# Kernel optimization log

Measured on AMD Instinct MI355X. Metric: run time of the kernel, lower is better.

Reference implementation:

```python
import jax, jax.numpy as jnp
import numpy as np

N, D, P = 4096, 1024, 2048
TAU, ALPHA = 0.2, 0.8
GAMMA_EX, GAMMA_IN = 2.0, 1.6
EPS = 1e-8


def _cos_sim(e):
    # F.cosine_similarity(e[:,None], e[None,:], dim=2) == normalized rows matmul
    n = jnp.linalg.norm(e, axis=1, keepdims=True)
    en = e / jnp.maximum(n, EPS)
    return en @ en.T  # [N, N]


def setup_inputs() -> dict:
    key = jax.random.key(0)
    embeddings = jax.random.normal(key, (N, D), dtype=jnp.float32)
    # positive pairs: (0,1),(2,3),... (arange fill)
    pp = np.arange(2 * P).reshape(P, 2)
    pos_partner = np.arange(N)
    pos_partner[pp[:, 0]] = pp[:, 1]
    pos_partner[pp[:, 1]] = pp[:, 0]
    # negative pairs = all ordered (i,j), i!=j, minus ordered positive tuples,
    # enumerated row-major (deterministic stand-in for torch's set order).
    pos_m = np.zeros((N, N), dtype=bool)
    pos_m[pp[:, 0], pp[:, 1]] = True
    neg_m = ~np.eye(N, dtype=bool) & ~pos_m
    ii, jj = np.nonzero(neg_m)  # row-major order
    neg_partner = np.arange(N)
    neg_partner[ii] = jj
    neg_partner[jj] = ii  # processed[j] = ... overwrites after
    return {
        "embeddings": embeddings,
        "positive_pairs": jnp.asarray(pp, jnp.int32),
        "pos_partner": jnp.asarray(pos_partner, jnp.int32),
        "neg_partner": jnp.asarray(neg_partner, jnp.int32),
    }


def reference(embeddings, positive_pairs, pos_partner, neg_partner):
    pi, pj = positive_pairs[:, 0], positive_pairs[:, 1]
    # Beta(gamma,gamma) scalar mixing coefficients (dim_mixing=False)
    lam_pos = jax.random.beta(jax.random.key(1), GAMMA_EX, GAMMA_EX) + 1.0  # 'ex'
    lam_neg = jax.random.beta(jax.random.key(2), GAMMA_IN, GAMMA_IN)        # 'in'

    orig = _cos_sim(embeddings)
    hp = _cos_sim(lam_pos * embeddings + (1.0 - lam_pos) * embeddings[pos_partner])
    hn = _cos_sim(lam_neg * embeddings + (1.0 - lam_neg) * embeddings[neg_partner])

    eye = jnp.eye(N, dtype=bool)
    pos_m = jnp.zeros((N, N), dtype=bool).at[pi, pj].set(True)  # ordered positives
    neg_m = ~eye & ~pos_m                                        # ordered negatives
    # pos replacement first, then neg replacement overwrites (faithful ordering)
    sim = jnp.where(pos_m | pos_m.T, hp, orig)
    sim = jnp.where(neg_m | neg_m.T, hn, sim)

    # ----- compute_loss (stage='train': quantile hard-negative mining) -----
    mask = eye | pos_m | pos_m.T
    exp_sim = jnp.exp(sim / TAU)
    exp_masked = jnp.where(mask, 0.0, exp_sim)
    pos_ij = exp_sim[pi, pj]
    pos_ji = exp_sim[pj, pi]
    exp_i = exp_masked[pi]  # [P, N]
    exp_j = exp_masked[pj]
    thr_i = jnp.quantile(exp_i, ALPHA, axis=1, keepdims=True)
    thr_j = jnp.quantile(exp_j, ALPHA, axis=1, keepdims=True)
    sum_i = jnp.where(exp_i >= thr_i, exp_i, 0.0).sum(axis=1)
    sum_j = jnp.where(exp_j >= thr_j, exp_j, 0.0).sum(axis=1)
    loss_ij = -jnp.log(pos_ij / (pos_ij + sum_i))
    loss_ji = -jnp.log(pos_ji / (pos_ji + sum_j))
    return (loss_ij + loss_ji).sum() / (2 * P)
```

## Files before the change

### kernel.cpp

```cpp
#include <hip/hip_runtime.h>
#include <hip/hip_bf16.h>

#define NN 4096
#define DD 1024
constexpr float LAM = 0.45f;
constexpr float INV_TAU = 5.0f;
constexpr int KSEL = 820;
constexpr unsigned KEY_BASE = 0x3B80u;
constexpr int NBINS = 2048;

typedef __attribute__((ext_vector_type(8))) short bf16x8;
typedef __attribute__((ext_vector_type(4))) float f32x4;

__device__ inline void async_copy16(const ushort* g, ushort* l) {
    __builtin_amdgcn_global_load_lds(
        (const __attribute__((address_space(1))) void*)g,
        (__attribute__((address_space(3))) void*)l, 16, 0, 0);
}

__global__ __launch_bounds__(256) void mixnorm_kernel(const float* __restrict__ E,
                                                      const int* __restrict__ negp,
                                                      ushort* __restrict__ U) {
    int r = blockIdx.x, t = threadIdx.x;
    int p = negp[r];
    const float a = LAM, b = 1.0f - LAM;
    float4 x = ((const float4*)(E + (size_t)r * DD))[t];
    float4 y = ((const float4*)(E + (size_t)p * DD))[t];
    float4 m;
    m.x = a * x.x + b * y.x;
    m.y = a * x.y + b * y.y;
    m.z = a * x.z + b * y.z;
    m.w = a * x.w + b * y.w;
    float ss = m.x * m.x + m.y * m.y + m.z * m.z + m.w * m.w;
    #pragma unroll
    for (int off = 32; off > 0; off >>= 1) ss += __shfl_down(ss, off, 64);
    __shared__ float part[4];
    if ((t & 63) == 0) part[t >> 6] = ss;
    __syncthreads();
    float tot = part[0] + part[1] + part[2] + part[3];
    float inv = 1.0f / fmaxf(sqrtf(tot), 1e-8f);
    ushort4 o;
    o.x = __bfloat16_as_ushort(__float2bfloat16(m.x * inv));
    o.y = __bfloat16_as_ushort(__float2bfloat16(m.y * inv));
    o.z = __bfloat16_as_ushort(__float2bfloat16(m.z * inv));
    o.w = __bfloat16_as_ushort(__float2bfloat16(m.w * inv));
    ((ushort4*)(U + (size_t)r * DD))[t] = o;
}

__global__ __launch_bounds__(512) void gemm_exp_kernel(const ushort* __restrict__ U,
                                                       ushort* __restrict__ Z) {
    __shared__ ushort sm_all[10240];
    ushort* As = sm_all;
    ushort* Bs = sm_all + 4096;
    const int t = threadIdx.x;
    const int w = t >> 6, l = t & 63;

    const int m = blockIdx.x;
    float fdec = sqrtf(8.0f * (float)m + 1.0f);
    int by = (int)((fdec - 1.0f) * 0.5f);
    while ((by + 1) * (by + 2) / 2 <= m) by++;
    while (by * (by + 1) / 2 > m) by--;
    const int bx = m - by * (by + 1) / 2;

    const ushort* gA = U + (size_t)(by * 128 + (t >> 2)) * DD + (t & 3) * 8;
    const ushort* gB = U + (size_t)(bx * 128 + (t >> 2)) * DD + (t & 3) * 8;
    ushort* lA = As + w * 512;
    ushort* lB = Bs + w * 512;

    f32x4 acc[2][4];
    #pragma unroll
    for (int i = 0; i < 2; i++)
        #pragma unroll
        for (int j = 0; j < 4; j++) acc[i][j] = (f32x4){0.f, 0.f, 0.f, 0.f};

    const int wr = w >> 1, wc = w & 1;
    const int mrow = wr * 32 + (l & 15);
    const int nrow = wc * 64 + (l & 15);
    const int kq = (l >> 4) * 8;

    for (int k0 = 0; k0 < DD; k0 += 32) {
        async_copy16(gA, lA);
        async_copy16(gB, lB);
        gA += 32; gB += 32;
        __syncthreads();
        bf16x8 af[2], bfr[4];
        #pragma unroll
        for (int i = 0; i < 2; i++)
            af[i] = *(const bf16x8*)(As + (mrow + i * 16) * 32 + kq);
        #pragma unroll
        for (int j = 0; j < 4; j++)
            bfr[j] = *(const bf16x8*)(Bs + (nrow + j * 16) * 32 + kq);
        __syncthreads();
        #pragma unroll
        for (int i = 0; i < 2; i++)
            #pragma unroll
            for (int j = 0; j < 4; j++)
                acc[i][j] = __builtin_amdgcn_mfma_f32_16x16x32_bf16(af[i], bfr[j], acc[i][j], 0, 0, 0);
    }

    ushort* smv = sm_all;
    ushort* smT = sm_all + 4096;
    const bool mirror = (bx != by);
    #pragma unroll
    for (int h = 0; h < 4; h++) {
        __syncthreads();
        if (wr == h) {
            #pragma unroll
            for (int i = 0; i < 2; i++)
                #pragma unroll
                for (int j = 0; j < 4; j++)
                    #pragma unroll
                    for (int rg = 0; rg < 4; rg++) {
                        float v = __expf(acc[i][j][rg] * INV_TAU);
                        ushort hv = __bfloat16_as_ushort(__float2bfloat16(v));
                        int lrow = i * 16 + ((l >> 4) << 2) + rg;
                        int lcol = (wc << 6) + j * 16 + (l & 15);
                        smv[lrow * 128 + lcol] = hv;
                        smT[lcol * 48 + lrow] = hv;
                    }
        }
        __syncthreads();
        {
            const uint4* src = (const uint4*)(smv + (t >> 4) * 128 + (t & 15) * 8);
            uint4* dst = (uint4*)(Z + (size_t)(by * 128 + h * 32 + (t >> 4)) * NN + bx * 128 + (t & 15) * 8);
            *dst = *src;
        }
        if (mirror) {
            const uint4* srcT = (const uint4*)(smT + (t >> 2) * 48 + (t & 3) * 8);
            uint4* dstT = (uint4*)(Z + (size_t)(bx * 128 + (t >> 2)) * NN + by * 128 + h * 32 + (t & 3) * 8);
            *dstT = *srcT;
        }
    }
}

__global__ __launch_bounds__(256) void rowloss_kernel(const ushort* __restrict__ Z,
                                                      const int* __restrict__ posp,
                                                      float* __restrict__ loss) {
    __shared__ unsigned histall[4][NBINS / 2];
    const int t = threadIdx.x, w = t >> 6, l = t & 63;
    const int r = blockIdx.x * 4 + w;
    unsigned* hist = histall[w];
    const int p = posp[r];
    const uint4* zr = (const uint4*)(Z + (size_t)r * NN);

    #pragma unroll
    for (int q = 0; q < 4; q++) ((uint4*)hist)[l * 4 + q] = (uint4){0u, 0u, 0u, 0u};

    const float posv = __uint_as_float(((unsigned)Z[(size_t)r * NN + p]) << 16);

    #pragma unroll 4
    for (int c = 0; c < 16; c++) {
        uint4 v = zr[c * 64 + l];
        unsigned wd[4] = {v.x, v.y, v.z, v.w};
        const int cb = (c * 64 + l) * 8;
        #pragma unroll
        for (int q = 0; q < 4; q++) {
            unsigned lo = wd[q] & 0xFFFFu;
            unsigned hi = wd[q] >> 16;
            int c0 = cb + 2 * q, c1 = c0 + 1;
            lo = (c0 == p || c0 == r) ? 0u : lo;
            hi = (c1 == p || c1 == r) ? 0u : hi;
            int b0 = max(0, min(NBINS - 1, (int)lo - (int)KEY_BASE));
            int b1 = max(0, min(NBINS - 1, (int)hi - (int)KEY_BASE));
            atomicAdd(&hist[b0 >> 1], 1u << ((b0 & 1) * 16));
            atomicAdd(&hist[b1 >> 1], 1u << ((b1 & 1) * 16));
        }
    }

    unsigned ow[16];
    {
        const uint4* hv = (const uint4*)(hist + l * 16);
        #pragma unroll
        for (int q = 0; q < 4; q++) {
            uint4 x = hv[q];
            ow[4 * q] = x.x; ow[4 * q + 1] = x.y; ow[4 * q + 2] = x.z; ow[4 * q + 3] = x.w;
        }
    }
    unsigned lsum = 0;
    #pragma unroll
    for (int i = 0; i < 16; i++) lsum += (ow[i] & 0xFFFFu) + (ow[i] >> 16);
    unsigned S = lsum;
    #pragma unroll
    for (int d = 1; d < 64; d <<= 1) {
        unsigned o = __shfl_down(S, d, 64);
        if (l + d < 64) S += o;
    }
    const bool cross = (S >= (unsigned)KSEL) && (S - lsum) < (unsigned)KSEL;
    int bstar = 0;
    if (cross) {
        int rem = KSEL - (int)(S - lsum);
        int a2 = 0;
        #pragma unroll
        for (int i = 31; i >= 0; i--) {
            unsigned c = (ow[i >> 1] >> ((i & 1) * 16)) & 0xFFFFu;
            a2 += (int)c;
            if (a2 >= rem) { bstar = l * 32 + i; break; }
        }
    }
    unsigned long long bm = __ballot(cross);
    int src = __ffsll((long long)bm) - 1;
    bstar = __shfl(bstar, src, 64);

    float s = 0.f;
    #pragma unroll
    for (int i = 0; i < 32; i++) {
        int g = l * 32 + i;
        unsigned c = (ow[i >> 1] >> ((i & 1) * 16)) & 0xFFFFu;
        if (g >= bstar && c) {
            float val = __uint_as_float((KEY_BASE + (unsigned)g) << 16);
            s = fmaf((float)c, val, s);
        }
    }
    #pragma unroll
    for (int off = 32; off > 0; off >>= 1) s += __shfl_down(s, off, 64);
    if (l == 0) loss[r] = log1pf(s / posv);
}

__global__ __launch_bounds__(256) void finalize_kernel(const float* __restrict__ loss,
                                                       unsigned* __restrict__ out) {
    __shared__ float part[4];
    const int t = threadIdx.x, w = t >> 6, l = t & 63;
    float s = 0.f;
    #pragma unroll
    for (int q = 0; q < 4; q++) {
        float4 v = ((const float4*)loss)[t * 4 + q];
        s += (v.x + v.y) + (v.z + v.w);
    }
    #pragma unroll
    for (int off = 32; off > 0; off >>= 1) s += __shfl_down(s, off, 64);
    if (l == 0) part[w] = s;
    __syncthreads();
    if (t == 0) {
        float v = (part[0] + part[1] + part[2] + part[3]) * (1.0f / 4096.0f);
        unsigned short bits = __bfloat16_as_ushort(__float2bfloat16(v));
        *out = ((unsigned)bits << 16) | (unsigned)bits;
    }
}

extern "C" void kernel_launch(void* const* d_in, const int* in_sizes, int n_in,
                              void* d_out, int out_size, void* d_ws, size_t ws_size,
                              hipStream_t stream) {
    const float* E = (const float*)d_in[0];
    const int* posp = (const int*)d_in[2];
    const int* negp = (const int*)d_in[3];

    float* loss = (float*)d_ws;
    ushort* U = (ushort*)((char*)d_ws + 16384);
    ushort* Z = (ushort*)((char*)d_ws + 16384 + (size_t)NN * DD * 2);

    mixnorm_kernel<<<NN, 256, 0, stream>>>(E, negp, U);
    gemm_exp_kernel<<<528, 512, 0, stream>>>(U, Z);
    rowloss_kernel<<<NN / 4, 256, 0, stream>>>(Z, posp, loss);
    finalize_kernel<<<1, 256, 0, stream>>>(loss, (unsigned*)d_out);
}
```

Before: 129.4 us.

## Double-buffer LDS tiles in gemm_exp_kernel to overlap global loads with MFMA

The K loop now keeps two LDS buffers for the A and B tiles. It issues the async global-to-LDS copy for the next 32-wide K slice before running MFMAs on the current slice. This cuts the barriers per K step from two to one and lets memory latency hide behind compute. In exchange, shared memory per block grows from about 20 KB to 32 KB, which could lower occupancy. It also relies on the barrier waiting for outstanding async loads.

```diff
diff --git a/kernel.cpp b/kernel.cpp
--- a/kernel.cpp
+++ b/kernel.cpp
@@ -49,9 +49,11 @@
 
 __global__ __launch_bounds__(512) void gemm_exp_kernel(const ushort* __restrict__ U,
                                                        ushort* __restrict__ Z) {
-    __shared__ ushort sm_all[10240];
-    ushort* As = sm_all;
-    ushort* Bs = sm_all + 4096;
+    __shared__ ushort sm_all[16384];
+    ushort* A0 = sm_all;
+    ushort* B0 = sm_all + 4096;
+    ushort* A1 = sm_all + 8192;
+    ushort* B1 = sm_all + 12288;
     const int t = threadIdx.x;
     const int w = t >> 6, l = t & 63;
 
@@ -64,8 +66,10 @@
 
     const ushort* gA = U + (size_t)(by * 128 + (t >> 2)) * DD + (t & 3) * 8;
     const ushort* gB = U + (size_t)(bx * 128 + (t >> 2)) * DD + (t & 3) * 8;
-    ushort* lA = As + w * 512;
-    ushort* lB = Bs + w * 512;
+    ushort* lA0 = A0 + w * 512;
+    ushort* lB0 = B0 + w * 512;
+    ushort* lA1 = A1 + w * 512;
+    ushort* lB1 = B1 + w * 512;
 
     f32x4 acc[2][4];
     #pragma unroll
@@ -78,24 +82,51 @@
     const int nrow = wc * 64 + (l & 15);
     const int kq = (l >> 4) * 8;
 
-    for (int k0 = 0; k0 < DD; k0 += 32) {
-        async_copy16(gA, lA);
-        async_copy16(gB, lB);
-        gA += 32; gB += 32;
-        __syncthreads();
-        bf16x8 af[2], bfr[4];
-        #pragma unroll
-        for (int i = 0; i < 2; i++)
-            af[i] = *(const bf16x8*)(As + (mrow + i * 16) * 32 + kq);
-        #pragma unroll
-        for (int j = 0; j < 4; j++)
-            bfr[j] = *(const bf16x8*)(Bs + (nrow + j * 16) * 32 + kq);
-        __syncthreads();
-        #pragma unroll
-        for (int i = 0; i < 2; i++)
+    async_copy16(gA, lA0);
+    async_copy16(gB, lB0);
+    gA += 32; gB += 32;
+
+    for (int k0 = 0; k0 < DD; k0 += 64) {
+        __syncthreads();
+        {
+            async_copy16(gA, lA1);
+            async_copy16(gB, lB1);
+            gA += 32; gB += 32;
+        }
+        {
+            bf16x8 af[2], bfr[4];
+            #pragma unroll
+            for (int i = 0; i < 2; i++)
+                af[i] = *(const bf16x8*)(A0 + (mrow + i * 16) * 32 + kq);
             #pragma unroll
             for (int j = 0; j < 4; j++)
-                acc[i][j] = __builtin_amdgcn_mfma_f32_16x16x32_bf16(af[i], bfr[j], acc[i][j], 0, 0, 0);
+                bfr[j] = *(const bf16x8*)(B0 + (nrow + j * 16) * 32 + kq);
+            #pragma unroll
+            for (int i = 0; i < 2; i++)
+                #pragma unroll
+                for (int j = 0; j < 4; j++)
+                    acc[i][j] = __builtin_amdgcn_mfma_f32_16x16x32_bf16(af[i], bfr[j], acc[i][j], 0, 0, 0);
+        }
+        __syncthreads();
+        if (k0 + 64 < DD) {
+            async_copy16(gA, lA0);
+            async_copy16(gB, lB0);
+            gA += 32; gB += 32;
+        }
+        {
+            bf16x8 af[2], bfr[4];
+            #pragma unroll
+            for (int i = 0; i < 2; i++)
+                af[i] = *(const bf16x8*)(A1 + (mrow + i * 16) * 32 + kq);
+            #pragma unroll
+            for (int j = 0; j < 4; j++)
+                bfr[j] = *(const bf16x8*)(B1 + (nrow + j * 16) * 32 + kq);
+            #pragma unroll
+            for (int i = 0; i < 2; i++)
+                #pragma unroll
+                for (int j = 0; j < 4; j++)
+                    acc[i][j] = __builtin_amdgcn_mfma_f32_16x16x32_bf16(af[i], bfr[j], acc[i][j], 0, 0, 0);
+        }
     }
 
     ushort* smv = sm_all;
```

Result: slower. 137.2 us (+6.1%).
